# Kernel optimization log

Measured on AMD Instinct MI355X. Metric: run time of the kernel, lower is better.

## Reference

```python
import jax, jax.numpy as jnp
import numpy as np

N, H, P, L, E, F = 131072, 256, 32768, 16, 8, 16
FUSED = 3 * H + E + F  # 792


def setup_inputs() -> dict:
    key = jax.random.key(0)
    ks = jax.random.split(key, 8)
    return {
        "node_embs": jax.random.normal(ks[0], (N, H), jnp.float32),
        "path_nodes": jax.random.randint(ks[1], (P, L), 0, N),
        "path_lens": jax.random.randint(ks[2], (P,), 0, L + 1),
        "path_edge_feats": jax.random.normal(ks[3], (P, E), jnp.float32),
        "path_scalar_feats": jax.random.normal(ks[4], (P, F), jnp.float32),
        "W1": jax.random.normal(ks[5], (FUSED, H), jnp.float32) / np.float32(np.sqrt(FUSED)),
        "b1": jnp.zeros((H,), jnp.float32),
        "W2": jax.random.normal(ks[6], (H, 1), jnp.float32) / np.float32(np.sqrt(H)),
        "b2": jnp.zeros((1,), jnp.float32),
        "src_idx": 0,
        "dst_idx": 1,
    }


def reference(node_embs, path_nodes, path_lens, path_edge_feats, path_scalar_feats,
              W1, b1, W2, b2, src_idx, dst_idx):
    dt = node_embs.dtype
    # ragged per-path mean over node embeddings, padded to [P, L]
    mask = (jnp.arange(L)[None, :] < path_lens[:, None]).astype(dt)  # [P, L]
    gathered = node_embs[path_nodes]                                  # [P, L, H]
    denom = jnp.maximum(path_lens, 1).astype(dt)[:, None]             # [P, 1]
    path_emb = jnp.einsum('plh,pl->ph', gathered, mask) / denom       # [P, H]

    src = jnp.broadcast_to(node_embs[src_idx], (P, H))
    dst = jnp.broadcast_to(node_embs[dst_idx], (P, H))
    fused = jnp.concatenate([src, dst, path_emb, path_edge_feats, path_scalar_feats], axis=1)  # [P, FUSED]

    h = jax.nn.relu(fused @ W1 + b1)   # [P, H]
    q = (h @ W2 + b2)[:, 0]            # [P]
    # empty paths produce exactly 0.0, matching the torch branch
    return jnp.where(path_lens > 0, q, jnp.zeros((), dt))
```

## Files before the change

### kernel.cpp

```cpp
#include <hip/hip_runtime.h>

#define NN      131072
#define H       256
#define PPATHS  32768
#define LMAX    16
#define EF      8
#define FF      16
#define KP      288
#define TPB     32
#define FS      296

typedef short v8s __attribute__((ext_vector_type(8)));
typedef float v4f __attribute__((ext_vector_type(4)));

__device__ __forceinline__ unsigned short f2bf(float x) {
    unsigned int u = __float_as_uint(x);
    u += 0x7fffu + ((u >> 16) & 1u);
    return (unsigned short)(u >> 16);
}

__global__ __launch_bounds__(256) void prep_kernel(
        const float* __restrict__ node_embs,
        const float* __restrict__ W1,
        const float* __restrict__ b1,
        const int*   __restrict__ si,
        const int*   __restrict__ di,
        unsigned short* __restrict__ W1T,
        float*       __restrict__ cvec) {
    __shared__ float red[256];
    const int b = blockIdx.x;
    if (b < KP) {
        const int k = b, n = threadIdx.x;
        float v = 0.0f;
        if (k < 256)      v = W1[(size_t)(512 + k) * H + n];
        else if (k < 280) v = W1[(size_t)(768 + (k - 256)) * H + n];
        W1T[(size_t)n * KP + k] = f2bf(v);
    } else {
        const int jb = b - KP;
        const int t  = threadIdx.x;
        const int jl = t & 3, kp = t >> 2;
        const int j  = jb * 4 + jl;
        const float* src = node_embs + (size_t)si[0] * H;
        const float* dst = node_embs + (size_t)di[0] * H;
        float c = 0.0f;
        #pragma unroll
        for (int i = 0; i < 8; ++i) {
            int k = kp + i * 64;
            float f = (k < H) ? src[k] : dst[k - H];
            c += f * W1[(size_t)k * H + j];
        }
        red[t] = c;
        __syncthreads();
        for (int s = 128; s >= 4; s >>= 1) {
            if (t < s) red[t] += red[t + s];
            __syncthreads();
        }
        if (t < 4) cvec[jb * 4 + t] = b1[jb * 4 + t] + red[t];
    }
}

__global__ __launch_bounds__(256, 4) void fused_kernel(
        const float* __restrict__ node_embs,
        const int*   __restrict__ path_nodes,
        const int*   __restrict__ path_lens,
        const float* __restrict__ edge_f,
        const float* __restrict__ scal_f,
        const unsigned short* __restrict__ W1T,
        const float* __restrict__ cvec,
        const float* __restrict__ W2,
        const float* __restrict__ b2,
        float*       __restrict__ out) {
    __shared__ __align__(16) unsigned short feat[TPB * FS];
    __shared__ float qpart[TPB][5];

    const int tid  = threadIdx.x;
    const int wave = tid >> 6, lane = tid & 63;
    const int pb   = blockIdx.x * TPB;

    for (int i = tid; i < TPB * 32; i += 256) {
        const int p = i >> 5, s = i & 31;
        float v = 0.0f;
        if (s < EF)           v = edge_f[(size_t)(pb + p) * EF + s];
        else if (s < EF + FF) v = scal_f[(size_t)(pb + p) * FF + (s - EF)];
        feat[p * FS + H + s] = f2bf(v);
    }

    for (int pi = 0; pi < 8; ++pi) {
        const int p   = wave * 8 + pi;
        const int gp  = pb + p;
        const int len = path_lens[gp];
        const int iv  = path_nodes[(size_t)gp * LMAX + (lane & 15)];

        float4 a0 = make_float4(0, 0, 0, 0), a1 = make_float4(0, 0, 0, 0);
        float4 a2 = make_float4(0, 0, 0, 0), a3 = make_float4(0, 0, 0, 0);
        int l = 0;
        for (; l + 3 < len; l += 4) {
            const int n0 = __shfl(iv, l);
            const int n1 = __shfl(iv, l + 1);
            const int n2 = __shfl(iv, l + 2);
            const int n3 = __shfl(iv, l + 3);
            const float4 v0 = ((const float4*)(node_embs + (size_t)n0 * H))[lane];
            const float4 v1 = ((const float4*)(node_embs + (size_t)n1 * H))[lane];
            const float4 v2 = ((const float4*)(node_embs + (size_t)n2 * H))[lane];
            const float4 v3 = ((const float4*)(node_embs + (size_t)n3 * H))[lane];
            a0.x += v0.x; a0.y += v0.y; a0.z += v0.z; a0.w += v0.w;
            a1.x += v1.x; a1.y += v1.y; a1.z += v1.z; a1.w += v1.w;
            a2.x += v2.x; a2.y += v2.y; a2.z += v2.z; a2.w += v2.w;
            a3.x += v3.x; a3.y += v3.y; a3.z += v3.z; a3.w += v3.w;
        }
        for (; l < len; ++l) {
            const int n0 = __shfl(iv, l);
            const float4 v0 = ((const float4*)(node_embs + (size_t)n0 * H))[lane];
            a0.x += v0.x; a0.y += v0.y; a0.z += v0.z; a0.w += v0.w;
        }
        const float inv = 1.0f / (float)max(len, 1);
        ushort4 r;
        r.x = f2bf((a0.x + a1.x + a2.x + a3.x) * inv);
        r.y = f2bf((a0.y + a1.y + a2.y + a3.y) * inv);
        r.z = f2bf((a0.z + a1.z + a2.z + a3.z) * inv);
        r.w = f2bf((a0.w + a1.w + a2.w + a3.w) * inv);
        *(ushort4*)&feat[p * FS + 4 * lane] = r;
    }
    __syncthreads();

    const int col = lane & 15, quad = lane >> 4;
    const int n0  = wave * 64;

    v4f acc[2][4];
    float w2v[4];
    #pragma unroll
    for (int nt = 0; nt < 4; ++nt) {
        const float cv = cvec[n0 + nt * 16 + col];
        w2v[nt] = W2[n0 + nt * 16 + col];
        #pragma unroll
        for (int mt = 0; mt < 2; ++mt)
            acc[mt][nt] = (v4f){cv, cv, cv, cv};
    }

    const unsigned short* Alds  = feat + col * FS + quad * 8;
    const unsigned short* Bbase = W1T + (size_t)(n0 + col) * KP + quad * 8;

    for (int k0 = 0; k0 < KP; k0 += 32) {
        v8s a[2], b[4];
        #pragma unroll
        for (int mt = 0; mt < 2; ++mt)
            a[mt] = *(const v8s*)(Alds + mt * 16 * FS + k0);
        #pragma unroll
        for (int nt = 0; nt < 4; ++nt)
            b[nt] = *(const v8s*)(Bbase + (size_t)(nt * 16) * KP + k0);
        #pragma unroll
        for (int mt = 0; mt < 2; ++mt)
            #pragma unroll
            for (int nt = 0; nt < 4; ++nt)
                acc[mt][nt] = __builtin_amdgcn_mfma_f32_16x16x32_bf16(
                                  a[mt], b[nt], acc[mt][nt], 0, 0, 0);
    }

    #pragma unroll
    for (int mt = 0; mt < 2; ++mt) {
        float s[4];
        #pragma unroll
        for (int r = 0; r < 4; ++r) {
            float v = 0.0f;
            #pragma unroll
            for (int nt = 0; nt < 4; ++nt)
                v += fmaxf(acc[mt][nt][r], 0.0f) * w2v[nt];
            s[r] = v;
        }
        #pragma unroll
        for (int off = 1; off < 16; off <<= 1) {
            #pragma unroll
            for (int r = 0; r < 4; ++r)
                s[r] += __shfl_xor(s[r], off);
        }
        if (col == 0) {
            #pragma unroll
            for (int r = 0; r < 4; ++r)
                qpart[mt * 16 + quad * 4 + r][wave] = s[r];
        }
    }
    __syncthreads();

    if (tid < TPB) {
        const float q = qpart[tid][0] + qpart[tid][1] + qpart[tid][2] + qpart[tid][3] + b2[0];
        out[pb + tid] = (path_lens[pb + tid] > 0) ? q : 0.0f;
    }
}

extern "C" void kernel_launch(void* const* d_in, const int* in_sizes, int n_in,
                              void* d_out, int out_size, void* d_ws, size_t ws_size,
                              hipStream_t stream) {
    const float* node_embs  = (const float*)d_in[0];
    const int*   path_nodes = (const int*)d_in[1];
    const int*   path_lens  = (const int*)d_in[2];
    const float* edge_f     = (const float*)d_in[3];
    const float* scal_f     = (const float*)d_in[4];
    const float* W1         = (const float*)d_in[5];
    const float* b1         = (const float*)d_in[6];
    const float* W2         = (const float*)d_in[7];
    const float* b2         = (const float*)d_in[8];
    const int*   si         = (const int*)d_in[9];
    const int*   di         = (const int*)d_in[10];
    float* out = (float*)d_out;

    float*          cvec = (float*)d_ws;
    unsigned short* W1T  = (unsigned short*)((char*)d_ws + 1024);

    hipLaunchKernelGGL(prep_kernel, dim3(KP + 64), dim3(256), 0, stream,
                       node_embs, W1, b1, si, di, W1T, cvec);
    hipLaunchKernelGGL(fused_kernel, dim3(PPATHS / TPB), dim3(256), 0, stream,
                       node_embs, path_nodes, path_lens, edge_f, scal_f,
                       W1T, cvec, W2, b2, out);
}
```

Measured before the change: 233.3 us.

## Double-buffer path gathers through LDS with asynchronous global_load_lds

Rewrites the per-path embedding gather so each wave issues all 16 node-row loads for a path straight into a per-wave LDS staging buffer with global_load_lds. Two paths are kept in flight and reduced from LDS, with explicit vmcnt waits. This aims to raise memory-level parallelism and hide gather latency. The cost is about 147KB of dynamic LDS, which forces one block per CU instead of four. It also issues dummy loads of row 0 for short paths, and gathering can no longer overlap with another block's MFMA phase.

```diff
diff --git a/kernel.cpp b/kernel.cpp
--- a/kernel.cpp
+++ b/kernel.cpp
@@ -9,6 +9,11 @@
 #define KP      288
 #define TPB     32
 #define FS      296
+
+#define STAGE_BYTES (4 * 2 * 16 * 1024)
+#define FEAT_OFF    STAGE_BYTES
+#define QPART_OFF   (FEAT_OFF + TPB * FS * 2)
+#define SMEM_BYTES  (QPART_OFF + TPB * 5 * 4)
 
 typedef short v8s __attribute__((ext_vector_type(8)));
 typedef float v4f __attribute__((ext_vector_type(4)));
@@ -59,7 +64,37 @@
     }
 }
 
-__global__ __launch_bounds__(256, 4) void fused_kernel(
+__device__ __forceinline__ void issue_path(const float* __restrict__ ne,
+                                           float* sbuf, int ivv, int lenS, int lane) {
+    #pragma unroll
+    for (int l = 0; l < 16; ++l) {
+        const int n  = __builtin_amdgcn_readlane(ivv, l);
+        const int nn = (l < lenS) ? n : 0;
+        const float* g = ne + (size_t)nn * H + lane * 4;
+        __builtin_amdgcn_global_load_lds(
+            (const __attribute__((address_space(1))) void*)g,
+            (__attribute__((address_space(3))) void*)(sbuf + l * 256),
+            16, 0, 0);
+    }
+}
+
+__device__ __forceinline__ void consume_path(const float* sbuf, int lenS, int lane,
+                                             unsigned short* featrow) {
+    float4 a = make_float4(0, 0, 0, 0);
+    for (int l = 0; l < lenS; ++l) {
+        const float4 v = *(const float4*)(sbuf + l * 256 + lane * 4);
+        a.x += v.x; a.y += v.y; a.z += v.z; a.w += v.w;
+    }
+    const float inv = 1.0f / (float)max(lenS, 1);
+    ushort4 r;
+    r.x = f2bf(a.x * inv);
+    r.y = f2bf(a.y * inv);
+    r.z = f2bf(a.z * inv);
+    r.w = f2bf(a.w * inv);
+    *(ushort4*)(featrow + 4 * lane) = r;
+}
+
+__global__ __launch_bounds__(256, 1) void fused_kernel(
         const float* __restrict__ node_embs,
         const int*   __restrict__ path_nodes,
         const int*   __restrict__ path_lens,
@@ -70,8 +105,10 @@
         const float* __restrict__ W2,
         const float* __restrict__ b2,
         float*       __restrict__ out) {
-    __shared__ __align__(16) unsigned short feat[TPB * FS];
-    __shared__ float qpart[TPB][5];
+    extern __shared__ __align__(16) char smem[];
+    float*          stage = (float*)smem;
+    unsigned short* feat  = (unsigned short*)(smem + FEAT_OFF);
+    float*          qpart = (float*)(smem + QPART_OFF);
 
     const int tid  = threadIdx.x;
     const int wave = tid >> 6, lane = tid & 63;
@@ -85,41 +122,29 @@
         feat[p * FS + H + s] = f2bf(v);
     }
 
+    int lens[8], ivr[8];
+    #pragma unroll
     for (int pi = 0; pi < 8; ++pi) {
-        const int p   = wave * 8 + pi;
-        const int gp  = pb + p;
-        const int len = path_lens[gp];
-        const int iv  = path_nodes[(size_t)gp * LMAX + (lane & 15)];
-
-        float4 a0 = make_float4(0, 0, 0, 0), a1 = make_float4(0, 0, 0, 0);
-        float4 a2 = make_float4(0, 0, 0, 0), a3 = make_float4(0, 0, 0, 0);
-        int l = 0;
-        for (; l + 3 < len; l += 4) {
-            const int n0 = __shfl(iv, l);
-            const int n1 = __shfl(iv, l + 1);
-            const int n2 = __shfl(iv, l + 2);
-            const int n3 = __shfl(iv, l + 3);
-            const float4 v0 = ((const float4*)(node_embs + (size_t)n0 * H))[lane];
-            const float4 v1 = ((const float4*)(node_embs + (size_t)n1 * H))[lane];
-            const float4 v2 = ((const float4*)(node_embs + (size_t)n2 * H))[lane];
-            const float4 v3 = ((const float4*)(node_embs + (size_t)n3 * H))[lane];
-            a0.x += v0.x; a0.y += v0.y; a0.z += v0.z; a0.w += v0.w;
-            a1.x += v1.x; a1.y += v1.y; a1.z += v1.z; a1.w += v1.w;
-            a2.x += v2.x; a2.y += v2.y; a2.z += v2.z; a2.w += v2.w;
-            a3.x += v3.x; a3.y += v3.y; a3.z += v3.z; a3.w += v3.w;
-        }
-        for (; l < len; ++l) {
-            const int n0 = __shfl(iv, l);
-            const float4 v0 = ((const float4*)(node_embs + (size_t)n0 * H))[lane];
-            a0.x += v0.x; a0.y += v0.y; a0.z += v0.z; a0.w += v0.w;
-        }
-        const float inv = 1.0f / (float)max(len, 1);
-        ushort4 r;
-        r.x = f2bf((a0.x + a1.x + a2.x + a3.x) * inv);
-        r.y = f2bf((a0.y + a1.y + a2.y + a3.y) * inv);
-        r.z = f2bf((a0.z + a1.z + a2.z + a3.z) * inv);
-        r.w = f2bf((a0.w + a1.w + a2.w + a3.w) * inv);
-        *(ushort4*)&feat[p * FS + 4 * lane] = r;
+        const int gp = pb + wave * 8 + pi;
+        lens[pi] = __builtin_amdgcn_readfirstlane(path_lens[gp]);
+        ivr[pi]  = path_nodes[(size_t)gp * LMAX + (lane & 15)];
+    }
+    float* sb0 = stage + wave * 8192;
+    float* sb1 = sb0 + 4096;
+
+    asm volatile("s_waitcnt vmcnt(0)" ::: "memory");
+    issue_path(node_embs, sb0, ivr[0], lens[0], lane);
+    issue_path(node_embs, sb1, ivr[1], lens[1], lane);
+    #pragma unroll
+    for (int pi = 0; pi < 8; ++pi) {
+        if (pi < 7) { asm volatile("s_waitcnt vmcnt(16)" ::: "memory"); }
+        else        { asm volatile("s_waitcnt vmcnt(0)"  ::: "memory"); }
+        __builtin_amdgcn_sched_barrier(0);
+        float* sb = (pi & 1) ? sb1 : sb0;
+        consume_path(sb, lens[pi], lane, feat + (wave * 8 + pi) * FS);
+        __builtin_amdgcn_sched_barrier(0);
+        if (pi + 2 < 8)
+            issue_path(node_embs, sb, ivr[pi + 2], lens[pi + 2], lane);
     }
     __syncthreads();
 
@@ -176,13 +201,14 @@
         if (col == 0) {
             #pragma unroll
             for (int r = 0; r < 4; ++r)
-                qpart[mt * 16 + quad * 4 + r][wave] = s[r];
+                qpart[(mt * 16 + quad * 4 + r) * 5 + wave] = s[r];
         }
     }
     __syncthreads();
 
     if (tid < TPB) {
-        const float q = qpart[tid][0] + qpart[tid][1] + qpart[tid][2] + qpart[tid][3] + b2[0];
+        const float q = qpart[tid * 5 + 0] + qpart[tid * 5 + 1]
+                      + qpart[tid * 5 + 2] + qpart[tid * 5 + 3] + b2[0];
         out[pb + tid] = (path_lens[pb + tid] > 0) ? q : 0.0f;
     }
 }
@@ -206,9 +232,12 @@
     float*          cvec = (float*)d_ws;
     unsigned short* W1T  = (unsigned short*)((char*)d_ws + 1024);
 
+    hipFuncSetAttribute((const void*)fused_kernel,
+                        hipFuncAttributeMaxDynamicSharedMemorySize, SMEM_BYTES);
+
     hipLaunchKernelGGL(prep_kernel, dim3(KP + 64), dim3(256), 0, stream,
                        node_embs, W1, b1, si, di, W1T, cvec);
-    hipLaunchKernelGGL(fused_kernel, dim3(PPATHS / TPB), dim3(256), 0, stream,
+    hipLaunchKernelGGL(fused_kernel, dim3(PPATHS / TPB), dim3(256), SMEM_BYTES, stream,
                        node_embs, path_nodes, path_lens, edge_f, scal_f,
                        W1T, cvec, W2, b2, out);
 }
```

Result: slower. 258.2 us (+10.7%).
